# Optimization experiments

Hardware: AMD Instinct MI355X
Metric: run time of the kernel (lower is better)

Reference implementation:

```python
import jax, jax.numpy as jnp
import numpy as np

H = 4          # attention heads
K = 16         # knn neighbors
EPS = 1e-5     # BatchNorm eps


def setup_inputs() -> dict:
    key = jax.random.key(0)
    ks = jax.random.split(key, 10)
    B, C, T, N = 2, 128, 32, 512
    OUT = 128
    HID = 2 * C + 2 * OUT  # ff hidden = in*2 + out*2
    s = 0.02
    return {
        "x_all": jax.random.normal(ks[0], (B, C, T, N), jnp.float32),
        "Wq": jax.random.normal(ks[1], (C, C), jnp.float32) * s,
        "Wk": jax.random.normal(ks[2], (C, C), jnp.float32) * s,
        "Wv": jax.random.normal(ks[3], (C, C), jnp.float32) * s,
        "W1": jax.random.normal(ks[4], (HID, C), jnp.float32) * s,
        "W2": jax.random.normal(ks[5], (OUT, HID), jnp.float32) * s,
        "bn_gamma": 1.0 + 0.1 * jax.random.normal(ks[6], (OUT,), jnp.float32),
        "bn_beta": 0.1 * jax.random.normal(ks[7], (OUT,), jnp.float32),
        "bn_mean": 0.1 * jax.random.normal(ks[8], (OUT,), jnp.float32),
        "bn_var": jax.random.uniform(ks[9], (OUT,), jnp.float32, 0.5, 1.5),
    }


def reference(x_all, Wq, Wk, Wv, W1, W2, bn_gamma, bn_beta, bn_mean, bn_var):
    B, C, T, N = x_all.shape
    D = C // H
    # --- st_group_points: candidate pool = 3 consecutive frames (replicate temporal pad), frame-major ---
    xp = jnp.concatenate([x_all[:, :, :1], x_all, x_all[:, :, -1:]], axis=2)   # (B,C,T+2,N)
    pool = jnp.stack([xp[:, :, :-2], xp[:, :, 1:-1], xp[:, :, 2:]], axis=3)    # (B,C,T,3,N)
    pool = pool.reshape(B, C, T, 3 * N)                                        # (B,C,T,3N)
    # KNN on xyz (channels 0:3); sqrt is monotone so topk on squared dists gives same indices
    a = x_all[:, :3]                                                           # (B,3,T,N)
    b = pool[:, :3]                                                            # (B,3,T,3N)
    d2 = jnp.sum((a[..., :, None] - b[..., None, :]) ** 2, axis=1)             # (B,T,N,3N)
    _, idx = jax.lax.top_k(-d2, K)                                             # (B,T,N,K) smallest-dist
    nb = jnp.take_along_axis(pool[:, :, :, None, :], idx[:, None], axis=-1)    # (B,C,T,N,K)
    rel = x_all[..., None] - nb                                                # diff grouping (B,C,T,N,K)
    # --- per-point local attention over K neighbors (1x1 convs == channel matmuls), all t at once ---
    q = jnp.einsum('oc,bctn->botn', Wq, x_all).reshape(B, H, D, T, N)
    k = jnp.einsum('oc,bctnk->botnk', Wk, rel).reshape(B, H, D, T, N, K)
    v = jnp.einsum('oc,bctnk->botnk', Wv, rel).reshape(B, H, D, T, N, K)
    energy = jnp.einsum('bhdtn,bhdtnk->bhtnk', q, k) / jnp.sqrt(jnp.float32(D))
    attn = jax.nn.softmax(energy, axis=-1)                                     # (B,H,T,N,K)
    agg = jnp.einsum('bhtnk,bhdtnk->bhdtn', attn, v).reshape(B, C, T, N)
    # --- residual + BatchNorm1d (eval mode, running stats) + conv feed-forward ---
    h = x_all + agg
    scale = (bn_gamma / jnp.sqrt(bn_var + EPS))[None, :, None, None]
    h = (h - bn_mean[None, :, None, None]) * scale + bn_beta[None, :, None, None]
    h = jax.nn.leaky_relu(jnp.einsum('oc,bctn->botn', W1, h), 0.2)
    y = jnp.einsum('oc,bctn->botn', W2, h)                                     # (B,OUT,T,N)
    return jnp.concatenate([x_all[:, :4], y], axis=1)                          # (B,4+OUT,T,N)
```

## Files before the change

### kernel.cpp

```cpp
#include <hip/hip_runtime.h>
#include <hip/hip_bf16.h>

typedef __hip_bfloat16 bf16;
typedef unsigned long long u64;
typedef __attribute__((ext_vector_type(8))) short short8;
typedef __attribute__((ext_vector_type(4))) float f32x4;

#define B_   2
#define C_   128
#define T_   32
#define N_   512
#define K_   16
#define HID_ 512
#define TN   (T_*N_)
#define PTS  (B_*T_*N_)

#define MFMA_BF16(a,b,c) __builtin_amdgcn_mfma_f32_16x16x32_bf16((a),(b),(c),0,0,0)

__device__ __forceinline__ float b2f(bf16 v){ return __bfloat162float(v); }
__device__ __forceinline__ bf16  f2b(float v){ return __float2bfloat16(v); }

__device__ __forceinline__ float ldc(const void* p, int i, bool f32) {
  return f32 ? ((const float*)p)[i] : b2f(((const bf16*)p)[i]);
}

__global__ __launch_bounds__(256) void convw_kernel(
    const void* __restrict__ x,
    const void* wq, const void* wk, const void* wv,
    const void* w1, const void* w2, const void* g, const void* bb,
    const void* m, const void* v,
    bf16* __restrict__ wqb, bf16* __restrict__ wkb, bf16* __restrict__ wvb,
    bf16* __restrict__ w1b, bf16* __restrict__ w2b,
    float* __restrict__ gf, float* __restrict__ bf_, float* __restrict__ mf,
    float* __restrict__ vf, int* __restrict__ flag)
{
  __shared__ int cnt;
  if (threadIdx.x == 0) cnt = 0;
  __syncthreads();
  const unsigned short* u = (const unsigned short*)x;
  int w = 0;
#pragma unroll
  for (int j = 0; j < 8; ++j) {
    unsigned short hv = u[threadIdx.x*8 + j];
    int e = (hv >> 7) & 0xFF;
    if (e >= 0x89) w++;
  }
  if (w) atomicAdd(&cnt, w);
  __syncthreads();
  bool f32 = (cnt > 32);
  if (blockIdx.x == 0 && threadIdx.x == 0) *flag = f32 ? 1 : 0;

  int i = blockIdx.x*256 + threadIdx.x;
  if (i < 16384) { wqb[i] = f2b(ldc(wq, i, f32)); return; } i -= 16384;
  if (i < 16384) { wkb[i] = f2b(ldc(wk, i, f32)); return; } i -= 16384;
  if (i < 16384) { wvb[i] = f2b(ldc(wv, i, f32)); return; } i -= 16384;
  if (i < 65536) { w1b[i] = f2b(ldc(w1, i, f32)); return; } i -= 65536;
  if (i < 65536) { w2b[i] = f2b(ldc(w2, i, f32)); return; } i -= 65536;
  if (i < 128)   { gf[i]  = ldc(g, i, f32); return; }       i -= 128;
  if (i < 128)   { bf_[i] = ldc(bb, i, f32); return; }      i -= 128;
  if (i < 128)   { mf[i]  = ldc(m, i, f32); return; }       i -= 128;
  if (i < 128)   { vf[i]  = ldc(v, i, f32); return; }
}

__device__ __forceinline__ void proj_gemm(const bf16* __restrict__ W,
                                          bf16 (*ys)[136],
                                          const short8 am[4][4],
                                          int mrow, int quad, int wave)
{
#pragma unroll
  for (int oi = 0; oi < 2; ++oi) {
    int ot = wave*2 + oi;
    f32x4 acc[4];
#pragma unroll
    for (int mt=0;mt<4;++mt) acc[mt] = (f32x4){0.f,0.f,0.f,0.f};
#pragma unroll
    for (int kq=0;kq<4;++kq) {
      short8 bfr = *(const short8*)&W[(ot*16+mrow)*C_ + kq*32 + quad*8];
#pragma unroll
      for (int mt=0;mt<4;++mt) acc[mt] = MFMA_BF16(am[mt][kq], bfr, acc[mt]);
    }
#pragma unroll
    for (int mt=0;mt<4;++mt)
#pragma unroll
      for (int r=0;r<4;++r)
        ys[mt*16 + quad*4 + r][ot*16 + mrow] = f2b(acc[mt][r]);
  }
}

__device__ __forceinline__ void tile_store128(bf16* __restrict__ dst,
                                              const bf16 (*ys)[136], int tid)
{
#pragma unroll
  for (int it=0; it<4; ++it) {
    int flat = (it*256 + tid)*8;
    int p = flat >> 7, c = flat & 127;
    *(short8*)&dst[(size_t)p*C_ + c] = *(const short8*)&ys[p][c];
  }
}

__global__ __launch_bounds__(256) void proj_kernel(
    const void* __restrict__ x, const int* __restrict__ flag,
    const bf16* __restrict__ wqb, const bf16* __restrict__ wkb, const bf16* __restrict__ wvb,
    bf16* __restrict__ xTb, bf16* QT, bf16* __restrict__ KT, bf16* __restrict__ VT)
{
  __shared__ bf16 xs [64][136];
  __shared__ bf16 ysK[64][136];
  __shared__ bf16 ysV[64][136];
  int tid = threadIdx.x;
  int p0  = blockIdx.x * 64;
  int b   = p0 >> 14; int tn0 = p0 & (TN-1);
  if (*flag) {
    const float* xbase = (const float*)x + (size_t)b*C_*TN + tn0;
#pragma unroll
    for (int it=0; it<32; ++it) {
      int i = it*256 + tid;
      int c = i >> 6, p = i & 63;
      xs[p][c] = f2b(xbase[(size_t)c*TN + p]);
    }
  } else {
    const bf16* xbase = (const bf16*)x + (size_t)b*C_*TN + tn0;
#pragma unroll
    for (int it=0; it<32; ++it) {
      int i = it*256 + tid;
      int c = i >> 6, p = i & 63;
      xs[p][c] = xbase[(size_t)c*TN + p];
    }
  }
  __syncthreads();
  tile_store128(xTb + (size_t)p0*C_, xs, tid);
  int lane = tid & 63, wave = tid >> 6;
  int mrow = lane & 15, quad = lane >> 4;
  short8 am[4][4];
#pragma unroll
  for (int mt=0;mt<4;++mt)
#pragma unroll
    for (int kq=0;kq<4;++kq)
      am[mt][kq] = *(const short8*)&xs[mt*16 + mrow][kq*32 + quad*8];
  __syncthreads();
  proj_gemm(wqb, xs,  am, mrow, quad, wave);
  proj_gemm(wkb, ysK, am, mrow, quad, wave);
  proj_gemm(wvb, ysV, am, mrow, quad, wave);
  __syncthreads();
  tile_store128(QT + (size_t)p0*C_, xs,  tid);
  tile_store128(KT + (size_t)p0*C_, ysK, tid);
  tile_store128(VT + (size_t)p0*C_, ysV, tid);
}

__device__ __forceinline__ u64 shflx64(u64 v, int m) {
  return (u64)__shfl_xor((long long)v, m, 64);
}
template<int W>
__device__ __forceinline__ u64 bitonic64w(u64 key, int lane) {
#pragma unroll
  for (int k = 2; k <= W; k <<= 1) {
#pragma unroll
    for (int j = k >> 1; j >= 1; j >>= 1) {
      u64 p = shflx64(key, j);
      bool keep_min = ((lane & k) == 0) == ((lane & j) == 0);
      key = ((p < key) == keep_min) ? p : key;
    }
  }
  return key;
}
__device__ __forceinline__ unsigned bitonic32u(unsigned key, int lane) {
#pragma unroll
  for (int k = 2; k <= 64; k <<= 1) {
#pragma unroll
    for (int j = k >> 1; j >= 1; j >>= 1) {
      unsigned p = (unsigned)__shfl_xor((int)key, j, 64);
      bool keep_min = ((lane & k) == 0) == ((lane & j) == 0);
      key = ((p < key) == keep_min) ? p : key;
    }
  }
  return key;
}

__global__ __launch_bounds__(512) void knn_kernel(const void* __restrict__ x,
                                                  const int* __restrict__ flag,
                                                  int* __restrict__ idxout)
{
  __shared__ float4 cand4[3*N_];
  __shared__ u64 surv[8][64];
  int tid = threadIdx.x;
  int blk = blockIdx.x;
  int row = blk >> 6;
  int b = row >> 5, t = row & 31;
  int ng = blk & 63;
  bool f32 = (*flag != 0);
#pragma unroll
  for (int q = 0; q < 3; ++q) {
    int tt = t - 1 + q; tt = tt < 0 ? 0 : (tt > T_-1 ? T_-1 : tt);
    size_t base = ((size_t)b*C_*T_ + tt)*(size_t)N_ + tid;
    float c0, c1, c2;
    if (f32) {
      const float* xp = (const float*)x;
      c0 = xp[base]; c1 = xp[base + (size_t)T_*N_]; c2 = xp[base + 2*(size_t)T_*N_];
    } else {
      const bf16* xp = (const bf16*)x;
      c0 = b2f(xp[base]); c1 = b2f(xp[base + (size_t)T_*N_]); c2 = b2f(xp[base + 2*(size_t)T_*N_]);
    }
    cand4[q*N_ + tid] = make_float4(c0, c1, c2, 0.f);
  }
  __syncthreads();
  int wave = tid >> 6, lane = tid & 63;
  int n = ng*8 + wave;
  float4 a = cand4[N_ + n];
  unsigned db[24];
#pragma unroll
  for (int j = 0; j < 24; ++j) {
    float4 cm = cand4[lane + (j << 6)];
    float dx = a.x - cm.x;
    float dy = a.y - cm.y;
    float dz = a.z - cm.z;
    float d2 = __fadd_rn(__fadd_rn(__fmul_rn(dx,dx), __fmul_rn(dy,dy)), __fmul_rn(dz,dz));
    db[j] = __float_as_uint(d2);
  }
  unsigned bd = db[0];
#pragma unroll
  for (int j = 1; j < 24; ++j) bd = (db[j] < bd) ? db[j] : bd;
  unsigned sd = bitonic32u(bd, lane);
  unsigned U = (unsigned)__shfl((int)sd, 15, 64);
  int c = 0;
#pragma unroll
  for (int j = 0; j < 24; ++j) c += (db[j] <= U) ? 1 : 0;
  int sc = c;
#pragma unroll
  for (int d = 1; d < 64; d <<= 1) {
    int pv = __shfl_up(sc, d, 64);
    if (lane >= d) sc += pv;
  }
  int total = __shfl(sc, 63, 64);
  int ofs = sc - c;
  u64 out16;
  if (total <= 64) {
#pragma unroll
    for (int j = 0; j < 24; ++j) {
      if (db[j] <= U) {
        surv[wave][ofs] = ((u64)db[j] << 32) | (unsigned)(lane + (j << 6));
        ++ofs;
      }
    }
    __threadfence_block();
    u64 kk = (lane < total) ? surv[wave][lane] : ~0ull;
    out16 = (total <= 32) ? bitonic64w<32>(kk, lane)
                          : bitonic64w<64>(kk, lane);
  } else {
    u64 key[24];
#pragma unroll
    for (int j = 0; j < 24; ++j)
      key[j] = ((u64)db[j] << 32) | (unsigned)(lane + (j << 6));
    u64 res = ~0ull;
#pragma unroll 1
    for (int r = 0; r < 16; ++r) {
      u64 m2 = key[0];
#pragma unroll
      for (int j = 1; j < 24; ++j) m2 = (key[j] < m2) ? key[j] : m2;
#pragma unroll
      for (int s = 32; s >= 1; s >>= 1) {
        u64 p = shflx64(m2, s);
        m2 = (p < m2) ? p : m2;
      }
      if (lane == r) res = m2;
      int mwin = (int)(m2 & 0xffffffffu);
      int sel = ((mwin & 63) == lane) ? (mwin >> 6) : -1;
#pragma unroll
      for (int j = 0; j < 24; ++j) if (j == sel) key[j] = ~0ull;
    }
    out16 = res;
  }
  int point = (b*T_ + t)*N_ + n;
  if (lane < K_) idxout[point*K_ + lane] = (int)(out16 & 0xffffffffu);
}

__global__ __launch_bounds__(512) void attn_kernel(
    const int* __restrict__ idxin, const bf16* __restrict__ xTb,
    bf16* qhT , const bf16* __restrict__ KT,
    const bf16* __restrict__ VT,
    const float* __restrict__ gf, const float* __restrict__ bf_,
    const float* __restrict__ mf, const float* __restrict__ vf)
{
  __shared__ int   col_lds[4][16];
  __shared__ float qbuf[4][C_];
  __shared__ bf16  kbuf[4][K_][136];
  __shared__ bf16  vbuf[4][K_][136];
  __shared__ float e_lds[4][4][16];
  int tid = threadIdx.x;
  int pt = tid >> 7, o = tid & 127;
  int point = blockIdx.x*4 + pt;
  int b = point >> 14; int tn = point & (TN-1); int t = tn >> 9;
  if (o < K_) {
    int m = idxin[point*K_ + o];
    int j = m >> 9, nn = m & (N_-1);
    int tt = t-1+j; tt = tt<0?0:(tt>T_-1?T_-1:tt);
    col_lds[pt][o] = ((b*T_ + tt)*N_ + nn)*C_;
  }
  int self = point*C_;
  qbuf[pt][o] = b2f(qhT[self + o]);
  __syncthreads();
#pragma unroll
  for (int it = 0; it < 2; ++it) {
    int i = it*512 + tid;
    int pp = i >> 8, rem = i & 255, k = rem >> 4, ch = rem & 15;
    int src = col_lds[pp][k] + ch*8;
    *(short8*)&kbuf[pp][k][ch*8] = *(const short8*)&KT[src];
    *(short8*)&vbuf[pp][k][ch*8] = *(const short8*)&VT[src];
  }
  __syncthreads();
  if (tid < 256) {
    int pp = tid >> 6, j = tid & 63, hd = j >> 4, k = j & 15;
    const float* qp = &qbuf[pp][hd*32];
    const bf16*  kp = &kbuf[pp][k][hd*32];
    float e = 0.f;
#pragma unroll
    for (int d=0; d<32; ++d) e = fmaf(qp[d], b2f(kp[d]), e);
    e_lds[pp][hd][k] = -e * 0.17677669529663687f;
  }
  __syncthreads();
  int hd = o >> 5;
  float e[16]; float mx = -3e38f;
#pragma unroll
  for (int k=0;k<K_;++k){ e[k]=e_lds[pt][hd][k]; mx=fmaxf(mx,e[k]); }
  float ssum=0.f;
#pragma unroll
  for (int k=0;k<K_;++k){ e[k]=__expf(e[k]-mx); ssum+=e[k]; }
  float inv = 1.f/ssum;
  float acc = b2f(VT[self + o]);
#pragma unroll
  for (int k=0;k<K_;++k)
    acc = fmaf(-(e[k]*inv), b2f(vbuf[pt][k][o]), acc);
  float hv = b2f(xTb[self + o]) + acc;
  float sc = gf[o] / sqrtf(vf[o] + 1e-5f);
  qhT[self + o] = f2b((hv - mf[o])*sc + bf_[o]);
}

__global__ __launch_bounds__(256) void mlp_kernel(const bf16* __restrict__ hT,
                                                  const bf16* __restrict__ w1b,
                                                  const bf16* __restrict__ w2b,
                                                  const void* __restrict__ x,
                                                  const int* __restrict__ flag,
                                                  void* out)
{
  __shared__ bf16  hs[64][136];
  __shared__ bf16  hid[64][520];
  __shared__ float yf[64][133];
  int tid = threadIdx.x;
  int p0 = blockIdx.x*64;
  int lane = tid & 63, wave = tid >> 6;
  int mrow = lane & 15, quad = lane >> 4;
  bool f32o = (*flag != 0);
  {
    int c = tid >> 6, p = tid & 63;
    int pnt = p0 + p;
    int bb = pnt >> 14, tn = pnt & (TN-1);
    size_t si = ((size_t)bb*C_ + c)*TN + tn;
    size_t di = ((size_t)bb*132 + c)*TN + tn;
    if (f32o) ((float*)out)[di] = ((const float*)x)[si];
    else      ((bf16*)out)[di] = ((const bf16*)x)[si];
  }
#pragma unroll
  for (int it=0; it<4; ++it) {
    int flat = (it*256 + tid)*8;
    int p = flat >> 7, c = flat & 127;
    *(short8*)&hs[p][c] = *(const short8*)&hT[(size_t)(p0+p)*C_ + c];
  }
  __syncthreads();
  {
    short8 am[4][4];
#pragma unroll
    for (int mt=0;mt<4;++mt)
#pragma unroll
      for (int kq=0;kq<4;++kq)
        am[mt][kq] = *(const short8*)&hs[mt*16 + mrow][kq*32 + quad*8];
    for (int ot = wave*8; ot < wave*8 + 8; ++ot) {
      f32x4 acc[4];
#pragma unroll
      for (int mt=0;mt<4;++mt) acc[mt] = (f32x4){0.f,0.f,0.f,0.f};
#pragma unroll
      for (int kq=0;kq<4;++kq) {
        short8 bfr = *(const short8*)&w1b[(ot*16+mrow)*C_ + kq*32 + quad*8];
#pragma unroll
        for (int mt=0;mt<4;++mt) acc[mt] = MFMA_BF16(am[mt][kq], bfr, acc[mt]);
      }
#pragma unroll
      for (int mt=0;mt<4;++mt)
#pragma unroll
        for (int r=0;r<4;++r) {
          float z = acc[mt][r];
          hid[mt*16 + quad*4 + r][ot*16 + mrow] = f2b(z > 0.f ? z : 0.2f*z);
        }
    }
  }
  __syncthreads();
  {
    short8 ha[16];
#pragma unroll
    for (int ks=0;ks<16;++ks)
      ha[ks] = *(const short8*)&hid[wave*16 + mrow][ks*32 + quad*8];
#pragma unroll
    for (int otp=0; otp<4; ++otp) {
      f32x4 acc0 = (f32x4){0.f,0.f,0.f,0.f};
      f32x4 acc1 = (f32x4){0.f,0.f,0.f,0.f};
#pragma unroll
      for (int ks=0;ks<16;++ks) {
        short8 b0 = *(const short8*)&w2b[((otp*2  )*16+mrow)*HID_ + ks*32 + quad*8];
        short8 b1 = *(const short8*)&w2b[((otp*2+1)*16+mrow)*HID_ + ks*32 + quad*8];
        acc0 = MFMA_BF16(ha[ks], b0, acc0);
        acc1 = MFMA_BF16(ha[ks], b1, acc1);
      }
#pragma unroll
      for (int r=0;r<4;++r) {
        yf[wave*16 + quad*4 + r][(otp*2  )*16 + mrow] = acc0[r];
        yf[wave*16 + quad*4 + r][(otp*2+1)*16 + mrow] = acc1[r];
      }
    }
  }
  __syncthreads();
  int p = tid & 63;
  int point = p0 + p;
  int b = point >> 14, tn = point & (TN-1);
  size_t obase = (size_t)b*132*TN + tn;
#pragma unroll
  for (int j = 0; j < 32; ++j) {
    int o = (tid >> 6)*32 + j;
    float vv = yf[p][o];
    size_t oi = obase + (size_t)(4+o)*TN;
    if (f32o) ((float*)out)[oi] = vv;
    else      ((bf16*)out)[oi] = f2b(vv);
  }
}

extern "C" void kernel_launch(void* const* d_in, const int* in_sizes, int n_in,
                              void* d_out, int out_size, void* d_ws, size_t ws_size,
                              hipStream_t stream)
{
  (void)in_sizes; (void)n_in; (void)out_size; (void)ws_size;
  const void* x = d_in[0];
  char* ws = (char*)d_ws;
  const size_t MB = (size_t)1<<20;
  bf16*  QT  = (bf16* )(ws + 0*MB);
  bf16*  KT  = (bf16* )(ws + 8*MB);
  bf16*  VT  = (bf16* )(ws + 16*MB);
  bf16*  xTb = (bf16* )(ws + 24*MB);
  int*   idxw= (int*  )(ws + 32*MB);
  bf16*  wqb = (bf16* )(ws + 34*MB);
  bf16*  wkb = (bf16* )(ws + 34*MB + 0x8000);
  bf16*  wvb = (bf16* )(ws + 34*MB + 0x10000);
  bf16*  w1b = (bf16* )(ws + 34*MB + 0x18000);
  bf16*  w2b = (bf16* )(ws + 34*MB + 0x38000);
  float* gf  = (float*)(ws + 34*MB + 0x58000);
  float* bf_ = (float*)(ws + 34*MB + 0x58200);
  float* mf  = (float*)(ws + 34*MB + 0x58400);
  float* vf  = (float*)(ws + 34*MB + 0x58600);
  int*  flag = (int*  )(ws + 34*MB + 0x58800);

  convw_kernel<<<dim3(706), dim3(256), 0, stream>>>(
      x, d_in[1], d_in[2], d_in[3], d_in[4], d_in[5],
      d_in[6], d_in[7], d_in[8], d_in[9],
      wqb, wkb, wvb, w1b, w2b, gf, bf_, mf, vf, flag);
  proj_kernel <<<dim3(PTS/64), dim3(256), 0, stream>>>(x, flag, wqb, wkb, wvb, xTb, QT, KT, VT);
  knn_kernel  <<<dim3(PTS/8), dim3(512), 0, stream>>>(x, flag, idxw);
  attn_kernel <<<dim3(PTS/4), dim3(512), 0, stream>>>(idxw, xTb, QT , KT, VT, gf, bf_, mf, vf);
  mlp_kernel  <<<dim3(PTS/64), dim3(256), 0, stream>>>(QT , w1b, w2b, x, flag, d_out);
}
```

Before: 214.2 us.

## Restructure MLP kernel into 32-point tiles with split hidden dim and direct register output

The MLP kernel now handles 32 points per block instead of 64. It computes the hidden layer in two halves of 256 channels, accumulating the second GEMM in registers across the halves, and writes results straight from the MFMA accumulators as vector stores. This removes the large LDS buffers (input tile, full hidden tile, fp32 output staging), which cuts LDS use and should raise occupancy, and it replaces the scattered scalar output writes with contiguous vector stores. In exchange, W1/W2 fragments are re-read from global memory by twice as many blocks, and the A operands now come from global memory instead of LDS.

```diff
diff --git a/kernel.cpp b/kernel.cpp
--- a/kernel.cpp
+++ b/kernel.cpp
@@ -340,92 +340,97 @@
                                                   const int* __restrict__ flag,
                                                   void* out)
 {
-  __shared__ bf16  hs[64][136];
-  __shared__ bf16  hid[64][520];
-  __shared__ float yf[64][133];
+  __shared__ bf16 hidh[32][264];
   int tid = threadIdx.x;
-  int p0 = blockIdx.x*64;
+  int p0 = blockIdx.x*32;
   int lane = tid & 63, wave = tid >> 6;
   int mrow = lane & 15, quad = lane >> 4;
   bool f32o = (*flag != 0);
-  {
-    int c = tid >> 6, p = tid & 63;
-    int pnt = p0 + p;
-    int bb = pnt >> 14, tn = pnt & (TN-1);
-    size_t si = ((size_t)bb*C_ + c)*TN + tn;
-    size_t di = ((size_t)bb*132 + c)*TN + tn;
+  int bb = p0 >> 14;
+  int tn0 = p0 & (TN-1);
+  if (tid < 128) {
+    int c = tid >> 5, p = tid & 31;
+    size_t si = ((size_t)bb*C_ + c)*TN + tn0 + p;
+    size_t di = ((size_t)bb*132 + c)*TN + tn0 + p;
     if (f32o) ((float*)out)[di] = ((const float*)x)[si];
-    else      ((bf16*)out)[di] = ((const bf16*)x)[si];
-  }
-#pragma unroll
-  for (int it=0; it<4; ++it) {
-    int flat = (it*256 + tid)*8;
-    int p = flat >> 7, c = flat & 127;
-    *(short8*)&hs[p][c] = *(const short8*)&hT[(size_t)(p0+p)*C_ + c];
-  }
-  __syncthreads();
-  {
-    short8 am[4][4];
-#pragma unroll
-    for (int mt=0;mt<4;++mt)
+    else      ((bf16*)out)[di]  = ((const bf16*)x)[si];
+  }
+  f32x4 acc2[2][2];
+#pragma unroll
+  for (int oi=0;oi<2;++oi)
+#pragma unroll
+    for (int mt=0;mt<2;++mt) acc2[oi][mt] = (f32x4){0.f,0.f,0.f,0.f};
+
+#pragma unroll
+  for (int half = 0; half < 2; ++half) {
+    if (half) __syncthreads();
+    short8 am[2][4];
+#pragma unroll
+    for (int mt=0;mt<2;++mt)
 #pragma unroll
       for (int kq=0;kq<4;++kq)
-        am[mt][kq] = *(const short8*)&hs[mt*16 + mrow][kq*32 + quad*8];
-    for (int ot = wave*8; ot < wave*8 + 8; ++ot) {
-      f32x4 acc[4];
-#pragma unroll
-      for (int mt=0;mt<4;++mt) acc[mt] = (f32x4){0.f,0.f,0.f,0.f};
+        am[mt][kq] = *(const short8*)&hT[(size_t)(p0 + mt*16 + mrow)*C_ + kq*32 + quad*8];
+#pragma unroll
+    for (int oi = 0; oi < 4; ++oi) {
+      int ot_g = half*16 + wave*4 + oi;
+      int otl  = wave*4 + oi;
+      f32x4 acc[2];
+#pragma unroll
+      for (int mt=0;mt<2;++mt) acc[mt] = (f32x4){0.f,0.f,0.f,0.f};
 #pragma unroll
       for (int kq=0;kq<4;++kq) {
-        short8 bfr = *(const short8*)&w1b[(ot*16+mrow)*C_ + kq*32 + quad*8];
-#pragma unroll
-        for (int mt=0;mt<4;++mt) acc[mt] = MFMA_BF16(am[mt][kq], bfr, acc[mt]);
+        short8 bfr = *(const short8*)&w1b[(ot_g*16+mrow)*C_ + kq*32 + quad*8];
+#pragma unroll
+        for (int mt=0;mt<2;++mt) acc[mt] = MFMA_BF16(am[mt][kq], bfr, acc[mt]);
       }
 #pragma unroll
-      for (int mt=0;mt<4;++mt)
+      for (int mt=0;mt<2;++mt)
 #pragma unroll
         for (int r=0;r<4;++r) {
           float z = acc[mt][r];
-          hid[mt*16 + quad*4 + r][ot*16 + mrow] = f2b(z > 0.f ? z : 0.2f*z);
+          hidh[mt*16 + quad*4 + r][otl*16 + mrow] = f2b(z > 0.f ? z : 0.2f*z);
         }
     }
-  }
-  __syncthreads();
-  {
-    short8 ha[16];
-#pragma unroll
-    for (int ks=0;ks<16;++ks)
-      ha[ks] = *(const short8*)&hid[wave*16 + mrow][ks*32 + quad*8];
-#pragma unroll
-    for (int otp=0; otp<4; ++otp) {
-      f32x4 acc0 = (f32x4){0.f,0.f,0.f,0.f};
-      f32x4 acc1 = (f32x4){0.f,0.f,0.f,0.f};
-#pragma unroll
-      for (int ks=0;ks<16;++ks) {
-        short8 b0 = *(const short8*)&w2b[((otp*2  )*16+mrow)*HID_ + ks*32 + quad*8];
-        short8 b1 = *(const short8*)&w2b[((otp*2+1)*16+mrow)*HID_ + ks*32 + quad*8];
-        acc0 = MFMA_BF16(ha[ks], b0, acc0);
-        acc1 = MFMA_BF16(ha[ks], b1, acc1);
+    __syncthreads();
+#pragma unroll
+    for (int kc = 0; kc < 4; ++kc) {
+      short8 ha[2][2];
+#pragma unroll
+      for (int mt=0;mt<2;++mt)
+#pragma unroll
+        for (int kk=0;kk<2;++kk)
+          ha[mt][kk] = *(const short8*)&hidh[mt*16 + mrow][(kc*2+kk)*32 + quad*8];
+#pragma unroll
+      for (int oi=0;oi<2;++oi) {
+        int ot2 = wave*2 + oi;
+#pragma unroll
+        for (int kk=0;kk<2;++kk) {
+          int ks_g = half*8 + kc*2 + kk;
+          short8 bfr = *(const short8*)&w2b[(ot2*16+mrow)*HID_ + ks_g*32 + quad*8];
+#pragma unroll
+          for (int mt=0;mt<2;++mt)
+            acc2[oi][mt] = MFMA_BF16(ha[mt][kk], bfr, acc2[oi][mt]);
+        }
       }
-#pragma unroll
-      for (int r=0;r<4;++r) {
-        yf[wave*16 + quad*4 + r][(otp*2  )*16 + mrow] = acc0[r];
-        yf[wave*16 + quad*4 + r][(otp*2+1)*16 + mrow] = acc1[r];
+    }
+  }
+  size_t obase = (size_t)bb*132*TN;
+#pragma unroll
+  for (int oi=0;oi<2;++oi) {
+    int ch = (wave*2+oi)*16 + mrow;
+#pragma unroll
+    for (int mt=0;mt<2;++mt) {
+      int tn = tn0 + mt*16 + quad*4;
+      size_t oidx = obase + (size_t)(4+ch)*TN + tn;
+      if (f32o) {
+        *(f32x4*)&((float*)out)[oidx] = acc2[oi][mt];
+      } else {
+        bf16 tmp[4];
+#pragma unroll
+        for (int r=0;r<4;++r) tmp[r] = f2b(acc2[oi][mt][r]);
+        *(u64*)&((bf16*)out)[oidx] = *(u64*)tmp;
       }
     }
-  }
-  __syncthreads();
-  int p = tid & 63;
-  int point = p0 + p;
-  int b = point >> 14, tn = point & (TN-1);
-  size_t obase = (size_t)b*132*TN + tn;
-#pragma unroll
-  for (int j = 0; j < 32; ++j) {
-    int o = (tid >> 6)*32 + j;
-    float vv = yf[p][o];
-    size_t oi = obase + (size_t)(4+o)*TN;
-    if (f32o) ((float*)out)[oi] = vv;
-    else      ((bf16*)out)[oi] = f2b(vv);
   }
 }
 
@@ -460,5 +465,5 @@
   proj_kernel <<<dim3(PTS/64), dim3(256), 0, stream>>>(x, flag, wqb, wkb, wvb, xTb, QT, KT, VT);
   knn_kernel  <<<dim3(PTS/8), dim3(512), 0, stream>>>(x, flag, idxw);
   attn_kernel <<<dim3(PTS/4), dim3(512), 0, stream>>>(idxw, xTb, QT , KT, VT, gf, bf_, mf, vf);
-  mlp_kernel  <<<dim3(PTS/64), dim3(256), 0, stream>>>(QT , w1b, w2b, x, flag, d_out);
-}
+  mlp_kernel  <<<dim3(PTS/32), dim3(256), 0, stream>>>(QT , w1b, w2b, x, flag, d_out);
+}
```

New measurement: 210.9 us. About the same (-1.6%).
